# Kernel optimization log

Hardware: AMD Instinct MI355X
Metric: run time of the kernel (lower is better)

The kernel has to match this reference:

```python
import jax, jax.numpy as jnp
import numpy as np

C = 256
CQK = C // 8


def setup_inputs() -> dict:
    key = jax.random.key(0)
    ks = jax.random.split(key, 8)
    B, H, W = 4, 64, 64
    inputs = jax.random.normal(ks[0], (B, H, W, C), dtype=jnp.float32)
    s = 1.0 / np.sqrt(C)
    Wq = jax.random.normal(ks[1], (C, CQK), dtype=jnp.float32) * s
    bq = jnp.zeros((CQK,), dtype=jnp.float32)
    Wk = jax.random.normal(ks[2], (C, CQK), dtype=jnp.float32) * s
    bk = jnp.zeros((CQK,), dtype=jnp.float32)
    Wv = jax.random.normal(ks[3], (C, C), dtype=jnp.float32) * s
    bv = jnp.zeros((C,), dtype=jnp.float32)
    gamma = jnp.float32(0.7)  # nonzero so attention branch contributes
    return {"inputs": inputs, "Wq": Wq, "bq": bq, "Wk": Wk, "bk": bk,
            "Wv": Wv, "bv": bv, "gamma": gamma}


def reference(inputs, Wq, bq, Wk, bk, Wv, bv, gamma):
    B, H, W, Cin = inputs.shape
    N = H * W
    x = inputs.reshape(B, N, Cin)
    # 1x1 convs == per-pixel channel matmuls
    q = x @ Wq + bq                      # (B, N, C//8)
    k = x @ Wk + bk                      # (B, N, C//8)
    v = x @ Wv + bv                      # (B, N, C)
    energy = jnp.einsum('bnd,bmd->bnm', q, k)   # (B, N, N), no scale (faithful)
    attn = jax.nn.softmax(energy, axis=-1)
    x_out = jnp.einsum('bnm,bmc->bnc', attn, v)  # (B, N, C)
    out = gamma * x_out.reshape(B, H, W, Cin) + inputs
    return out
```

## Files before the change

kernel.cpp:

```cpp
#include <hip/hip_runtime.h>
#include <hip/hip_bf16.h>

#define B_ 4
#define N_ 4096
#define C_ 256
#define D_ 32
#define LOG2E 1.44269504088896340736f
#define MFMA16 __builtin_amdgcn_mfma_f32_16x16x32_bf16

typedef __attribute__((ext_vector_type(8))) short short8;
typedef __attribute__((ext_vector_type(4))) short short4v;
typedef __attribute__((ext_vector_type(4))) float float4v;

__device__ inline short f2bf_rne(float f) {
  unsigned u = __builtin_bit_cast(unsigned, f);
  u += 0x7FFFu + ((u >> 16) & 1u);
  return (short)(u >> 16);
}
__device__ inline float bf2f(short s) {
  unsigned u = ((unsigned)(unsigned short)s) << 16;
  return __builtin_bit_cast(float, u);
}
__device__ inline float fast_exp2(float x) { return __builtin_amdgcn_exp2f(x); }

__device__ inline short4v pk4_bf16(float p0, float p1, float p2, float p3) {
  union { unsigned u[2]; short4v s; } r;
  asm("v_cvt_pk_bf16_f32 %0, %1, %2" : "=v"(r.u[0]) : "v"(p0), "v"(p1));
  asm("v_cvt_pk_bf16_f32 %0, %1, %2" : "=v"(r.u[1]) : "v"(p2), "v"(p3));
  return r.s;
}

__global__ __launch_bounds__(256) void cast_w_kernel(
    const float* __restrict__ Wq, const float* __restrict__ Wk,
    const float* __restrict__ Wv, short* __restrict__ WtF) {
  int i  = blockIdx.x * 256 + threadIdx.x;
  int j  = i & 7;
  int l  = (i >> 3) & 63;
  int ks = (i >> 9) & 7;
  int nb = i >> 12;
  int n  = nb * 16 + (l & 15);
  int k  = ks * 32 + ((l >> 4) << 3) + j;
  float v;
  if (n < 32)      v = Wq[k * 32 + n] * LOG2E;
  else if (n < 64) v = Wk[k * 32 + (n - 32)];
  else             v = Wv[k * 256 + (n - 64)];
  WtF[i] = f2bf_rne(v);
}

__global__ __launch_bounds__(256, 2) void proj_kernel(
    const float* __restrict__ x, const short* __restrict__ WtF,
    const float* __restrict__ bq, const float* __restrict__ bk,
    const float* __restrict__ bv,
    short* __restrict__ qb, short* __restrict__ kF, short* __restrict__ vF) {
  int blk = blockIdx.x;
  int b  = blk >> 7;
  int r0 = (blk & 127) * 32;
  int t  = threadIdx.x;
  int w  = t >> 6;
  int l  = t & 63;
  int lc = l & 15;
  int q4 = l >> 4;

  __shared__ __align__(16) short sA[32][272];
  __shared__ __align__(16) short sV[256][40];
  __shared__ __align__(16) short sK[32][36];

  {
    const float* xb = x + (size_t)(b * N_ + r0) * C_;
#pragma unroll
    for (int ch = 0; ch < 8; ch++) {
      int f   = ch * 256 + t;
      int row = f >> 6;
      int col = (f & 63) * 4;
      float4v v = *(const float4v*)(xb + f * 4);
      short4v s = pk4_bf16(v[0], v[1], v[2], v[3]);
      *(short4v*)(&sA[row][col]) = s;
    }
  }
  __syncthreads();

  float4v acc[10];
#pragma unroll
  for (int i = 0; i < 10; i++) { acc[i][0] = 0.f; acc[i][1] = 0.f; acc[i][2] = 0.f; acc[i][3] = 0.f; }

  const short* wbase = WtF + w * 4096 + l * 8;

#define LOADW(B0, B1, B2, B3, B4, KS)                       \
  B0 = *(const short8*)(wbase + (KS) * 512 + 0 * 16384);    \
  B1 = *(const short8*)(wbase + (KS) * 512 + 1 * 16384);    \
  B2 = *(const short8*)(wbase + (KS) * 512 + 2 * 16384);    \
  B3 = *(const short8*)(wbase + (KS) * 512 + 3 * 16384);    \
  B4 = *(const short8*)(wbase + (KS) * 512 + 4 * 16384);

#define DO_MFMA(A0, A1, B0, B1, B2, B3, B4)                 \
  acc[0] = MFMA16(A0, B0, acc[0], 0, 0, 0);                 \
  acc[1] = MFMA16(A1, B0, acc[1], 0, 0, 0);                 \
  acc[2] = MFMA16(A0, B1, acc[2], 0, 0, 0);                 \
  acc[3] = MFMA16(A1, B1, acc[3], 0, 0, 0);                 \
  acc[4] = MFMA16(A0, B2, acc[4], 0, 0, 0);                 \
  acc[5] = MFMA16(A1, B2, acc[5], 0, 0, 0);                 \
  acc[6] = MFMA16(A0, B3, acc[6], 0, 0, 0);                 \
  acc[7] = MFMA16(A1, B3, acc[7], 0, 0, 0);                 \
  acc[8] = MFMA16(A0, B4, acc[8], 0, 0, 0);                 \
  acc[9] = MFMA16(A1, B4, acc[9], 0, 0, 0);

  short8 wA0, wA1, wA2, wA3, wA4, wB0, wB1, wB2, wB3, wB4;
  LOADW(wA0, wA1, wA2, wA3, wA4, 0)
#pragma unroll
  for (int kk = 0; kk < 8; kk += 2) {
    short8 a00 = *(const short8*)(&sA[lc][kk * 32 + q4 * 8]);
    short8 a01 = *(const short8*)(&sA[16 + lc][kk * 32 + q4 * 8]);
    LOADW(wB0, wB1, wB2, wB3, wB4, kk + 1)
    DO_MFMA(a00, a01, wA0, wA1, wA2, wA3, wA4)
    short8 a10 = *(const short8*)(&sA[lc][(kk + 1) * 32 + q4 * 8]);
    short8 a11 = *(const short8*)(&sA[16 + lc][(kk + 1) * 32 + q4 * 8]);
    LOADW(wA0, wA1, wA2, wA3, wA4, kk + 2)
    DO_MFMA(a10, a11, wB0, wB1, wB2, wB3, wB4)
  }
#undef LOADW
#undef DO_MFMA

  {
    float bias0 = (w < 2) ? bq[w * 16 + lc] * LOG2E : bk[(w - 2) * 16 + lc];
#pragma unroll
    for (int rt = 0; rt < 2; rt++) {
      if (w < 2) {
#pragma unroll
        for (int r = 0; r < 4; r++) {
          int row = rt * 16 + q4 * 4 + r;
          qb[(size_t)(b * N_ + r0 + row) * D_ + w * 16 + lc] =
              f2bf_rne(acc[rt][r] + bias0);
        }
      } else {
#pragma unroll
        for (int r = 0; r < 4; r++) {
          int row = rt * 16 + q4 * 4 + r;
          sK[row][(w - 2) * 16 + lc] = f2bf_rne(acc[rt][r] + bias0);
        }
      }
    }
#pragma unroll
    for (int nbo = 1; nbo < 5; nbo++) {
      float bias = bv[(nbo - 1) * 64 + w * 16 + lc];
#pragma unroll
      for (int rt = 0; rt < 2; rt++) {
        float4v a = acc[nbo * 2 + rt];
        short4v pk = pk4_bf16(a[0] + bias, a[1] + bias, a[2] + bias, a[3] + bias);
        *(short4v*)(&sV[(nbo - 1) * 64 + w * 16 + lc][rt * 16 + q4 * 4]) = pk;
      }
    }
  }
  __syncthreads();

  int kt  = r0 >> 6;
  int ks0 = (r0 >> 5) & 1;

  {
    size_t tb2 = ((size_t)(b * 64 + kt) * 32 + ks0 * 16) * 512;
    int cb = t >> 4;
#pragma unroll
    for (int k = 0; k < 4; k++) {
      int p = (t & 15) * 4 + k;
      int j = p >> 4, i = p & 15;
      short8 vv = *(const short8*)(&sV[cb * 16 + i][j * 8]);
      *(short8*)(vF + tb2 + (size_t)t * 32 + k * 8) = vv;
    }
  }
  if (t < 128) {
    int fr = t >> 6, ll = t & 63;
    int kv = fr * 16 + (ll & 15), dg = ll >> 4;
    size_t tbk = ((size_t)(b * 64 + kt) * 4 + ks0 * 2) * 512;
    short8 kv8 = *(const short8*)(&sK[kv][dg * 8]);
    *(short8*)(kF + tbk + (size_t)t * 8) = kv8;
  }
}

__device__ __forceinline__ void barrier_lds_only() {
  asm volatile("s_waitcnt lgkmcnt(0)\n\ts_barrier" ::: "memory");
}

__global__ __launch_bounds__(512, 4) void flash_fused_kernel(
    const short* __restrict__ qb, const short* __restrict__ kF,
    const short* __restrict__ vF, const float* __restrict__ xin,
    const float* __restrict__ gptr, float* __restrict__ out) {
  int blk = blockIdx.x;
  int b  = blk & 3;
  int qt = blk >> 2;
  int r0 = qt * 64;
  int t  = threadIdx.x;
  int w  = t >> 6;
  int l  = t & 63;
  int lc = l & 15;
  int q4 = l >> 4;
  int rq = w & 3;
  int kh = w >> 2;

  __shared__ __align__(16) short sPn[2][4096];
  __shared__ float sL[4][16];
  __shared__ float sLinv[64];

  float g = *gptr;

  short8 qf = *(const short8*)(qb + (size_t)(b * N_ + r0 + rq * 16 + lc) * D_ + q4 * 8);

  const short* kbp = kF + ((size_t)(b * 64) * 4) * 512 + kh * 1024 + l * 8;
  const short* vbp = vF + ((size_t)(b * 64) * 32 + 2 * w) * 512 + l * 8;

  short8 kC0, kC1;
  short8 vX00, vX01, vX10, vX11;
  short8 vY00, vY01, vY10, vY11;

  kC0 = *(const short8*)(kbp + 0);
  kC1 = *(const short8*)(kbp + 512);
  vX00 = *(const short8*)(vbp + 0);
  vX01 = *(const short8*)(vbp + 512);
  vX10 = *(const short8*)(vbp + 8192);
  vX11 = *(const short8*)(vbp + 8704);

  float4v O[8];
#pragma unroll
  for (int i = 0; i < 8; i++) { O[i][0] = 0.f; O[i][1] = 0.f; O[i][2] = 0.f; O[i][3] = 0.f; }
  float l_part = 0.f;

  int qkbase = (rq * 2) * 512 + (((q4 >> 1) * 16) + lc) * 8 + (q4 & 1) * 4;

#define K_RELOAD(TI)                                                           \
  { size_t o_ = (size_t)(TI) * 2048;                                           \
    kC0 = *(const short8*)(kbp + o_);                                          \
    kC1 = *(const short8*)(kbp + o_ + 512); }

#define QK_STEP(SPB, VALID)                                                    \
  { __builtin_amdgcn_s_setprio(1);                                             \
    float4v z; z[0] = 0.f; z[1] = 0.f; z[2] = 0.f; z[3] = 0.f;                 \
    float4v S0 = MFMA16(kC0, qf, z, 0, 0, 0);                                  \
    float4v S1 = MFMA16(kC1, qf, z, 0, 0, 0);                                  \
    short* rowp = &sPn[SPB][qkbase + kh * 512];                                \
    float ts = 0.f;                                                            \
    { float p0 = fast_exp2(S0[0]), p1 = fast_exp2(S0[1]);                      \
      float p2 = fast_exp2(S0[2]), p3 = fast_exp2(S0[3]);                      \
      ts += (p0 + p1) + (p2 + p3);                                             \
      *(short4v*)(rowp + 0) = pk4_bf16(p0, p1, p2, p3); }                      \
    { float p0 = fast_exp2(S1[0]), p1 = fast_exp2(S1[1]);                      \
      float p2 = fast_exp2(S1[2]), p3 = fast_exp2(S1[3]);                      \
      ts += (p0 + p1) + (p2 + p3);                                             \
      *(short4v*)(rowp + 256) = pk4_bf16(p0, p1, p2, p3); }                    \
    __builtin_amdgcn_s_setprio(0);                                             \
    if (VALID) l_part += ts; }

#define PV_STEP(SPB, V00, V01, V10, V11)                                       \
  { _Pragma("unroll")                                                          \
    for (int rt = 0; rt < 4; rt++) {                                           \
      short8 pf0 = *(const short8*)(&sPn[SPB][(rt * 2 + 0) * 512 + l * 8]);    \
      short8 pf1 = *(const short8*)(&sPn[SPB][(rt * 2 + 1) * 512 + l * 8]);    \
      O[rt * 2 + 0] = MFMA16(pf0, V00, O[rt * 2 + 0], 0, 0, 0);                \
      O[rt * 2 + 0] = MFMA16(pf1, V10, O[rt * 2 + 0], 0, 0, 0);                \
      O[rt * 2 + 1] = MFMA16(pf0, V01, O[rt * 2 + 1], 0, 0, 0);                \
      O[rt * 2 + 1] = MFMA16(pf1, V11, O[rt * 2 + 1], 0, 0, 0);                \
    } }

  QK_STEP(0, true)
  K_RELOAD(1)
  barrier_lds_only();

  for (int ti = 0; ti < 64; ti += 2) {
    int n1 = ti + 1;
    int n2 = (ti + 2 < 64) ? ti + 2 : 63;
    bool v2 = (ti + 2 < 64);
    int n3 = (ti + 3 < 64) ? ti + 3 : 63;

    { size_t vo = (size_t)n1 * 16384;
      vY00 = *(const short8*)(vbp + vo);
      vY01 = *(const short8*)(vbp + vo + 512);
      vY10 = *(const short8*)(vbp + vo + 8192);
      vY11 = *(const short8*)(vbp + vo + 8704); }
    QK_STEP(1, true)
    K_RELOAD(n2)
    PV_STEP(0, vX00, vX01, vX10, vX11)
    barrier_lds_only();

    { size_t vo = (size_t)n2 * 16384;
      vX00 = *(const short8*)(vbp + vo);
      vX01 = *(const short8*)(vbp + vo + 512);
      vX10 = *(const short8*)(vbp + vo + 8192);
      vX11 = *(const short8*)(vbp + vo + 8704); }
    QK_STEP(0, v2)
    K_RELOAD(n3)
    PV_STEP(1, vY00, vY01, vY10, vY11)
    barrier_lds_only();
  }
#undef K_RELOAD
#undef QK_STEP
#undef PV_STEP

  {
    float l_tot = l_part + __shfl_xor(l_part, 16, 64);
    l_tot += __shfl_xor(l_tot, 32, 64);
    if (kh == 0 && q4 == 0) sL[rq][lc] = l_tot;
    __syncthreads();
    if (kh == 1 && q4 == 0)
      sLinv[rq * 16 + lc] = g * __builtin_amdgcn_rcpf(l_tot + sL[rq][lc]);
    __syncthreads();
  }

  {
#pragma unroll
    for (int a = 0; a < 8; a++) {
      int rt   = a >> 1;
      int cbo  = a & 1;
      int row0 = rt * 16 + q4 * 4;
      int chg  = w * 32 + cbo * 16 + lc;
      size_t gi = (size_t)(b * N_ + r0 + row0) * C_ + chg;
      const float* xp = xin + gi;
      float* op = out + gi;
      float4v o = O[a];
#pragma unroll
      for (int r = 0; r < 4; r++) {
        op[(size_t)r * C_] = o[r] * sLinv[row0 + r] + xp[(size_t)r * C_];
      }
    }
  }
}

extern "C" void kernel_launch(void* const* d_in, const int* in_sizes, int n_in,
                              void* d_out, int out_size, void* d_ws, size_t ws_size,
                              hipStream_t stream) {
  const float* x     = (const float*)d_in[0];
  const float* Wq    = (const float*)d_in[1];
  const float* bq    = (const float*)d_in[2];
  const float* Wk    = (const float*)d_in[3];
  const float* bk    = (const float*)d_in[4];
  const float* Wv    = (const float*)d_in[5];
  const float* bv    = (const float*)d_in[6];
  const float* gamma = (const float*)d_in[7];
  float* out = (float*)d_out;

  char* ws = (char*)d_ws;
  short* qb   = (short*)ws;
  short* kF   = (short*)(ws + (1u << 20));
  short* vF   = (short*)(ws + (2u << 20));
  short* WtF  = (short*)(ws + (10u << 20));

  hipLaunchKernelGGL(cast_w_kernel,      dim3(320), dim3(256), 0, stream, Wq, Wk, Wv, WtF);
  hipLaunchKernelGGL(proj_kernel,        dim3(512), dim3(256), 0, stream, x, WtF, bq, bk, bv, qb, kF, vF);
  hipLaunchKernelGGL(flash_fused_kernel, dim3(256), dim3(512), 0, stream, qb, kF, vF, x, gamma, out);
}
```

Measured before the change: 132.2 us.

## Halve query tile to 32 rows and double grid for more blocks

Each block now handles 32 query rows instead of 64, and the grid grows from 256 to 512 blocks. The eight waves are regrouped into 2 row groups × 2 key halves × 2 key sub-slices, so each wave runs one QK MFMA per tile instead of two and keeps half as many output accumulators. Row sums are combined across four waves through shared memory. The aim is to fill more CUs on the 256-CU part and to cut registers per wave, at the cost of reading K and V twice as often overall.

```diff
diff --git a/kernel.cpp b/kernel.cpp
--- a/kernel.cpp
+++ b/kernel.cpp
@@ -186,70 +186,61 @@
   int blk = blockIdx.x;
   int b  = blk & 3;
   int qt = blk >> 2;
-  int r0 = qt * 64;
+  int r0 = qt * 32;
   int t  = threadIdx.x;
   int w  = t >> 6;
   int l  = t & 63;
   int lc = l & 15;
   int q4 = l >> 4;
-  int rq = w & 3;
-  int kh = w >> 2;
-
-  __shared__ __align__(16) short sPn[2][4096];
-  __shared__ float sL[4][16];
-  __shared__ float sLinv[64];
+  int rq = w & 1;
+  int kh = (w >> 1) & 1;
+  int ks = w >> 2;
+
+  __shared__ __align__(16) short sPn[2][2048];
+  __shared__ float sL2[8][16];
+  __shared__ float sLinv[32];
 
   float g = *gptr;
 
   short8 qf = *(const short8*)(qb + (size_t)(b * N_ + r0 + rq * 16 + lc) * D_ + q4 * 8);
 
-  const short* kbp = kF + ((size_t)(b * 64) * 4) * 512 + kh * 1024 + l * 8;
+  const short* kbp = kF + ((size_t)(b * 64) * 4) * 512 + (kh * 2 + ks) * 512 + l * 8;
   const short* vbp = vF + ((size_t)(b * 64) * 32 + 2 * w) * 512 + l * 8;
 
-  short8 kC0, kC1;
+  short8 kC0;
   short8 vX00, vX01, vX10, vX11;
   short8 vY00, vY01, vY10, vY11;
 
   kC0 = *(const short8*)(kbp + 0);
-  kC1 = *(const short8*)(kbp + 512);
   vX00 = *(const short8*)(vbp + 0);
   vX01 = *(const short8*)(vbp + 512);
   vX10 = *(const short8*)(vbp + 8192);
   vX11 = *(const short8*)(vbp + 8704);
 
-  float4v O[8];
-#pragma unroll
-  for (int i = 0; i < 8; i++) { O[i][0] = 0.f; O[i][1] = 0.f; O[i][2] = 0.f; O[i][3] = 0.f; }
+  float4v O[4];
+#pragma unroll
+  for (int i = 0; i < 4; i++) { O[i][0] = 0.f; O[i][1] = 0.f; O[i][2] = 0.f; O[i][3] = 0.f; }
   float l_part = 0.f;
 
-  int qkbase = (rq * 2) * 512 + (((q4 >> 1) * 16) + lc) * 8 + (q4 & 1) * 4;
+  int qkbase = (rq * 2 + kh) * 512 + ks * 256 + (((q4 >> 1) * 16) + lc) * 8 + (q4 & 1) * 4;
 
 #define K_RELOAD(TI)                                                           \
-  { size_t o_ = (size_t)(TI) * 2048;                                           \
-    kC0 = *(const short8*)(kbp + o_);                                          \
-    kC1 = *(const short8*)(kbp + o_ + 512); }
+  { kC0 = *(const short8*)(kbp + (size_t)(TI) * 2048); }
 
 #define QK_STEP(SPB, VALID)                                                    \
   { __builtin_amdgcn_s_setprio(1);                                             \
     float4v z; z[0] = 0.f; z[1] = 0.f; z[2] = 0.f; z[3] = 0.f;                 \
     float4v S0 = MFMA16(kC0, qf, z, 0, 0, 0);                                  \
-    float4v S1 = MFMA16(kC1, qf, z, 0, 0, 0);                                  \
-    short* rowp = &sPn[SPB][qkbase + kh * 512];                                \
-    float ts = 0.f;                                                            \
-    { float p0 = fast_exp2(S0[0]), p1 = fast_exp2(S0[1]);                      \
-      float p2 = fast_exp2(S0[2]), p3 = fast_exp2(S0[3]);                      \
-      ts += (p0 + p1) + (p2 + p3);                                             \
-      *(short4v*)(rowp + 0) = pk4_bf16(p0, p1, p2, p3); }                      \
-    { float p0 = fast_exp2(S1[0]), p1 = fast_exp2(S1[1]);                      \
-      float p2 = fast_exp2(S1[2]), p3 = fast_exp2(S1[3]);                      \
-      ts += (p0 + p1) + (p2 + p3);                                             \
-      *(short4v*)(rowp + 256) = pk4_bf16(p0, p1, p2, p3); }                    \
+    short* rowp = &sPn[SPB][qkbase];                                           \
+    float p0 = fast_exp2(S0[0]), p1 = fast_exp2(S0[1]);                        \
+    float p2 = fast_exp2(S0[2]), p3 = fast_exp2(S0[3]);                        \
+    *(short4v*)(rowp) = pk4_bf16(p0, p1, p2, p3);                              \
     __builtin_amdgcn_s_setprio(0);                                             \
-    if (VALID) l_part += ts; }
+    if (VALID) l_part += (p0 + p1) + (p2 + p3); }
 
 #define PV_STEP(SPB, V00, V01, V10, V11)                                       \
   { _Pragma("unroll")                                                          \
-    for (int rt = 0; rt < 4; rt++) {                                           \
+    for (int rt = 0; rt < 2; rt++) {                                           \
       short8 pf0 = *(const short8*)(&sPn[SPB][(rt * 2 + 0) * 512 + l * 8]);    \
       short8 pf1 = *(const short8*)(&sPn[SPB][(rt * 2 + 1) * 512 + l * 8]);    \
       O[rt * 2 + 0] = MFMA16(pf0, V00, O[rt * 2 + 0], 0, 0, 0);                \
@@ -295,16 +286,18 @@
   {
     float l_tot = l_part + __shfl_xor(l_part, 16, 64);
     l_tot += __shfl_xor(l_tot, 32, 64);
-    if (kh == 0 && q4 == 0) sL[rq][lc] = l_tot;
+    if (q4 == 0) sL2[w][lc] = l_tot;
     __syncthreads();
-    if (kh == 1 && q4 == 0)
-      sLinv[rq * 16 + lc] = g * __builtin_amdgcn_rcpf(l_tot + sL[rq][lc]);
+    if (w < 2 && q4 == 0) {
+      float s = (sL2[w][lc] + sL2[w + 2][lc]) + (sL2[w + 4][lc] + sL2[w + 6][lc]);
+      sLinv[w * 16 + lc] = g * __builtin_amdgcn_rcpf(s);
+    }
     __syncthreads();
   }
 
   {
 #pragma unroll
-    for (int a = 0; a < 8; a++) {
+    for (int a = 0; a < 4; a++) {
       int rt   = a >> 1;
       int cbo  = a & 1;
       int row0 = rt * 16 + q4 * 4;
@@ -342,5 +335,5 @@
 
   hipLaunchKernelGGL(cast_w_kernel,      dim3(320), dim3(256), 0, stream, Wq, Wk, Wv, WtF);
   hipLaunchKernelGGL(proj_kernel,        dim3(512), dim3(256), 0, stream, x, WtF, bq, bk, bv, qb, kF, vF);
-  hipLaunchKernelGGL(flash_fused_kernel, dim3(256), dim3(512), 0, stream, qb, kF, vF, x, gamma, out);
-}
+  hipLaunchKernelGGL(flash_fused_kernel, dim3(512), dim3(512), 0, stream, qb, kF, vF, x, gamma, out);
+}
```

New measurement: 142.4 us. 1.08x slower.
